# Kernel tuning notes

Hardware: AMD Instinct MI355X
Metric: run time of the kernel (lower is better)

The kernel has to match this reference:

```python
import jax, jax.numpy as jnp
import numpy as np

H = 256
NUM_REL = 460
NUM_ENT = 20000
B = 4096
CUR_TS = 10
PATH_LEN = 8


def _gru_step(x, h, W_ih, W_hh, b_ih, b_hh):
    # PyTorch GRUCell math
    gi = x @ W_ih.T + b_ih          # [B, 3H]
    gh = h @ W_hh.T + b_hh          # [B, 3H]
    ir, iz, inn = jnp.split(gi, 3, axis=1)
    hr, hz, hn = jnp.split(gh, 3, axis=1)
    r = jax.nn.sigmoid(ir + hr)
    z = jax.nn.sigmoid(iz + hz)
    n = jnp.tanh(inn + r * hn)
    return (1.0 - z) * n + z * h


def setup_inputs() -> dict:
    key = jax.random.key(0)
    ks = jax.random.split(key, 24)
    s = 1.0 / np.sqrt(H)
    f32 = jnp.float32
    d = {
        "pre_emb": jax.random.normal(ks[0], (NUM_ENT, H), f32),
        "r_emb": jax.random.normal(ks[1], (NUM_REL, H), f32),
        "partial_embeding": jax.random.normal(ks[2], (B, CUR_TS * NUM_REL), f32),
        # params (uniform-ish linear init scaled by 1/sqrt(H))
        "W_map1": jax.random.normal(ks[3], (2 * H, H), f32) * s,
        "b_map1": jax.random.normal(ks[4], (2 * H,), f32) * s,
        "W_map2": jax.random.normal(ks[5], (H, 2 * H), f32) * s,
        "b_map2": jax.random.normal(ks[6], (H,), f32) * s,
        "W_h1": jax.random.normal(ks[7], (H, H), f32) * s,
        "b_h1": jax.random.normal(ks[8], (H,), f32) * s,
        "W_h2": jax.random.normal(ks[9], (H, H), f32) * s,
        "b_h2": jax.random.normal(ks[10], (H,), f32) * s,
        "W_attn": jax.random.normal(ks[11], (H, H), f32) * s,
        "b_attn": jax.random.normal(ks[12], (H,), f32) * s,
        "W_align": jax.random.normal(ks[13], (H, H), f32) * s,
        "b_align": jax.random.normal(ks[14], (H,), f32) * s,
        "W_ih": jax.random.normal(ks[15], (3 * H, H), f32) * s,
        "W_hh": jax.random.normal(ks[16], (3 * H, H), f32) * s,
        "b_ih": jax.random.normal(ks[17], (3 * H,), f32) * s,
        "b_hh": jax.random.normal(ks[18], (3 * H,), f32) * s,
        "all_triples": jax.random.randint(ks[19], (B, 3), 0, NUM_REL, dtype=jnp.int64)
        if jax.config.jax_enable_x64 else jax.random.randint(ks[19], (B, 3), 0, NUM_REL, dtype=jnp.int32),
        "cur_ts": CUR_TS,
        "num_rel": NUM_REL,
    }
    return d


def reference(pre_emb, r_emb, partial_embeding,
              W_map1, b_map1, W_map2, b_map2,
              W_h1, b_h1, W_h2, b_h2,
              W_attn, b_attn, W_align, b_align,
              W_ih, W_hh, b_ih, b_hh,
              all_triples, cur_ts, num_rel):
    # rel_mapping1 -> rel_mapping2
    mapped_rel = (r_emb @ W_map1.T + b_map1) @ W_map2.T + b_map2     # [R, H]
    q_rel = mapped_rel[all_triples[:, 1]]                            # [B, H]

    # attention logits base (constant over timesteps): linear_attn(q_rel) @ mapped_rel.T
    attn_base = (q_rel @ W_attn.T + b_attn) @ mapped_rel.T           # [B, R]

    start_ts = max(cur_ts - PATH_LEN, 0)
    nb = partial_embeding.shape[0]
    cur_seq = partial_embeding.reshape(nb, cur_ts, num_rel)[:, start_ts:cur_ts]  # [B, T, R]
    cur_seq = jnp.swapaxes(cur_seq, 0, 1)                            # [T, B, R]

    h0 = jnp.zeros((nb, H), dtype=pre_emb.dtype)

    def step(h, cur):
        attn = cur * attn_base
        attn = jnp.where(attn == 0, jnp.asarray(-1e9, attn.dtype), attn)
        attn = jax.nn.softmax(attn, axis=1)
        x = attn @ mapped_rel                                        # [B, H]
        return _gru_step(x, h, W_ih, W_hh, b_ih, b_hh), None

    gru_hidden, _ = jax.lax.scan(step, h0, cur_seq)

    # predicted history embedding + match loss (MSE)
    predicted_hist = 0.1 * ((q_rel @ W_h1.T + b_h1) @ W_h2.T + b_h2) + q_rel
    match_loss = jnp.mean((predicted_hist - gru_hidden) ** 2)

    # forward_forth, distmult scoring
    h2 = _gru_step(q_rel, predicted_hist, W_ih, W_hh, b_ih, b_hh)    # [B, H]
    aligned_all = pre_emb @ W_align.T + b_align                      # [E, H]
    sub = aligned_all[all_triples[:, 0]]                             # [B, H]
    score_logits = (sub * h2) @ aligned_all.T                        # [B, E]
    score = jax.nn.sigmoid(score_logits)

    # BCE(sigmoid(logits), one_hot(obj)) in stable logits form without
    # materializing the dense one-hot label matrix:
    # mean over B*E of [ softplus(x) - x * label ]
    obj = all_triples[:, 2]
    pos_logits = score_logits[jnp.arange(nb), obj]
    path_loss = (jnp.sum(jax.nn.softplus(score_logits)) - jnp.sum(pos_logits)) / (nb * score_logits.shape[1])

    return match_loss, path_loss, score
```

## Files before the change

### kernel.cpp

```cpp
#include <hip/hip_runtime.h>
#include <hip/hip_bf16.h>

typedef __hip_bfloat16 bf16;
typedef __attribute__((ext_vector_type(8))) short short8;
typedef __attribute__((ext_vector_type(4))) float f32x4;
typedef __attribute__((ext_vector_type(4))) short short4v;

#define NREL 460
#define KP   480
#define NENT 20000
#define NENT_PAD 20224
#define NB   4096

__device__ inline float sigmoidf_(float x){ return 1.f/(1.f+__expf(-x)); }

__device__ inline void gload16(const bf16* g, bf16* l){
  __builtin_amdgcn_global_load_lds(
      (const __attribute__((address_space(1))) unsigned int*)g,
      (__attribute__((address_space(3))) unsigned int*)l, 16, 0, 0);
}

__device__ __forceinline__ void fgemm_body(
    const float* __restrict__ A, int lda, int arows,
    const float* __restrict__ B, int ldb,
    const float* __restrict__ bias,
    float* __restrict__ C, int ldc, int K, int mode,
    const float* __restrict__ add_src, bf16* __restrict__ ct_out,
    float* As, float* Bs, int bx, int by)
{
  const int tid = threadIdx.x;
  const int row0 = bx*64, col0 = by*64;
  const int tx = tid & 15, ty = tid >> 4;
  float acc[4][4] = {};
  for (int k0 = 0; k0 < K; k0 += 32){
    __syncthreads();
    #pragma unroll
    for (int s = 0; s < 2; ++s){
      int slot = tid + s*256;
      int r = slot >> 3, c4 = (slot & 7)*4;
      int ra = row0 + r; if (ra >= arows) ra = arows - 1;
      float4 v = *(const float4*)(A + (long)ra*lda + k0 + c4);
      As[(c4+0)*68+r] = v.x; As[(c4+1)*68+r] = v.y; As[(c4+2)*68+r] = v.z; As[(c4+3)*68+r] = v.w;
      float4 w = *(const float4*)(B + (long)(col0 + r)*ldb + k0 + c4);
      Bs[(c4+0)*68+r] = w.x; Bs[(c4+1)*68+r] = w.y; Bs[(c4+2)*68+r] = w.z; Bs[(c4+3)*68+r] = w.w;
    }
    __syncthreads();
    #pragma unroll
    for (int kk = 0; kk < 32; ++kk){
      float4 a4 = *(const float4*)(&As[kk*68 + ty*4]);
      float4 b4 = *(const float4*)(&Bs[kk*68 + tx*4]);
      float av[4] = {a4.x, a4.y, a4.z, a4.w};
      float bv[4] = {b4.x, b4.y, b4.z, b4.w};
      #pragma unroll
      for (int i = 0; i < 4; ++i)
        #pragma unroll
        for (int j = 0; j < 4; ++j) acc[i][j] += av[i]*bv[j];
    }
  }
  const int rb = row0 + ty*4, cb = col0 + tx*4;
  if (mode == 1){
    #pragma unroll
    for (int i = 0; i < 4; ++i){
      float4 v = {acc[i][0], acc[i][1], acc[i][2], acc[i][3]};
      *(float4*)(C + (long)(rb+i)*ldc + cb) = v;
      int rr = rb + i;
      if (rr < KP){
        #pragma unroll
        for (int j = 0; j < 4; ++j)
          ct_out[(cb+j)*KP + rr] = __float2bfloat16(rr < NREL ? acc[i][j] : 0.f);
      }
    }
  } else if (mode == 2){
    #pragma unroll
    for (int i = 0; i < 4; ++i){
      float4 v;
      #pragma unroll
      for (int j = 0; j < 4; ++j)
        ((float*)&v)[j] = 0.1f*(acc[i][j] + bias[cb+j]) + add_src[(long)(rb+i)*ldc + cb+j];
      *(float4*)(C + (long)(rb+i)*ldc + cb) = v;
    }
  } else {
    float bv[4] = {0,0,0,0};
    if (bias){ bv[0]=bias[cb]; bv[1]=bias[cb+1]; bv[2]=bias[cb+2]; bv[3]=bias[cb+3]; }
    #pragma unroll
    for (int i = 0; i < 4; ++i){
      float4 v = {acc[i][0]+bv[0], acc[i][1]+bv[1], acc[i][2]+bv[2], acc[i][3]+bv[3]};
      *(float4*)(C + (long)(rb+i)*ldc + cb) = v;
    }
  }
}

struct FDesc {
  const float* A; const float* B; const float* bias; float* C;
  const float* add; bf16* ct;
  int lda, ldb, ldc, K, arows, mode;
};

template<int MODE>
__device__ __forceinline__ void gemm128_body(
    const bf16* __restrict__ A, int lda,
    const bf16* __restrict__ B, int ldb,
    const float* __restrict__ bias,
    void* __restrict__ C, long ldc,
    int K, int n_valid, double* __restrict__ sp_sum,
    const int* __restrict__ trips,
    bf16* sbuf, float* wsum, int bx, int by)
{
  const int tid = threadIdx.x;
  const int lane = tid & 63, wave = tid >> 6;
  const long row0 = (long)bx * 128;
  const long col0 = (long)by * 128;
  const int sr = tid >> 2;
  const int sc = ((tid & 3) ^ ((sr >> 1) & 3)) * 8;
  const bf16* Ag0 = A + (row0 + sr)*lda + sc;
  const bf16* Ag1 = A + (row0 + 64 + sr)*lda + sc;
  const bf16* Bg0 = B + (col0 + sr)*ldb + sc;
  const bf16* Bg1 = B + (col0 + 64 + sr)*ldb + sc;
  bf16* As_ = sbuf;
  bf16* Bs_ = sbuf + 12288;
  const int wr = (wave >> 1)*64, wc = (wave & 1)*64;
  const int rA = lane & 15;
  const int kA = ((lane >> 4) ^ ((rA >> 1) & 3)) * 8;
  f32x4 acc[4][4] = {};
  const int nt = K >> 5;
  auto stage = [&](int t, int buf){
    const int k0 = t << 5;
    gload16(Ag0 + k0, As_ + buf*4096 + tid*8);
    gload16(Ag1 + k0, As_ + buf*4096 + 2048 + tid*8);
    gload16(Bg0 + k0, Bs_ + buf*4096 + tid*8);
    gload16(Bg1 + k0, Bs_ + buf*4096 + 2048 + tid*8);
  };
  stage(0, 0); stage(1, 1);
  int cur = 0;
  for (int t = 0; t < nt; ++t){
    if (t + 2 < nt){
      int nb = cur + 2; if (nb >= 3) nb -= 3;
      stage(t + 2, nb);
      asm volatile("s_waitcnt vmcnt(8)" ::: "memory");
    } else if (t + 2 == nt){
      asm volatile("s_waitcnt vmcnt(4)" ::: "memory");
    } else {
      asm volatile("s_waitcnt vmcnt(0)" ::: "memory");
    }
    __builtin_amdgcn_s_barrier();
    short8 a[4], b[4];
    #pragma unroll
    for (int m = 0; m < 4; ++m) a[m] = *(const short8*)(As_ + cur*4096 + (wr + m*16 + rA)*32 + kA);
    #pragma unroll
    for (int n = 0; n < 4; ++n) b[n] = *(const short8*)(Bs_ + cur*4096 + (wc + n*16 + rA)*32 + kA);
    asm volatile("s_waitcnt lgkmcnt(0)" ::: "memory");
    __builtin_amdgcn_s_barrier();
    #pragma unroll
    for (int m = 0; m < 4; ++m)
      #pragma unroll
      for (int n = 0; n < 4; ++n)
        acc[m][n] = __builtin_amdgcn_mfma_f32_16x16x32_bf16(a[m], b[n], acc[m][n], 0,0,0);
    if (++cur == 3) cur = 0;
  }
  const int ri = (lane >> 4)*4, ci = lane & 15;
  __syncthreads();
  if constexpr (MODE == 1){
    bf16* epi = sbuf + wave*1152;
    const int rrow = lane >> 2, q = lane & 3;
    #pragma unroll
    for (int m = 0; m < 4; ++m){
      #pragma unroll
      for (int n = 0; n < 4; ++n){
        long c = col0 + wc + n*16 + ci;
        float bv = bias ? bias[c] : 0.f;
        #pragma unroll
        for (int i = 0; i < 4; ++i)
          epi[(ri+i)*72 + n*16 + ci] = __float2bfloat16(acc[m][n][i] + bv);
      }
      long gr = row0 + wr + m*16 + rrow;
      bf16* gp = (bf16*)C + gr*ldc + col0 + wc + q*16;
      const bf16* lp = epi + rrow*72 + q*16;
      *(short8*)(gp)     = *(const short8*)(lp);
      *(short8*)(gp + 8) = *(const short8*)(lp + 8);
    }
  } else {
    float* epi = (float*)sbuf + wave*1088;
    const int rrow = lane >> 2, q = lane & 3;
    const bool maybe = (col0 + wc) < 464;
    float spart = 0.f, ppart = 0.f;
    #pragma unroll
    for (int m = 0; m < 4; ++m){
      int obj[4];
      if (maybe){
        #pragma unroll
        for (int i = 0; i < 4; ++i)
          obj[i] = trips[3*(int)(row0 + wr + m*16 + ri + i) + 2];
      }
      #pragma unroll
      for (int n = 0; n < 4; ++n){
        long c = col0 + wc + n*16 + ci;
        bool cv = (c < n_valid);
        #pragma unroll
        for (int i = 0; i < 4; ++i){
          float v = acc[m][n][i];
          float sg = 0.f;
          if (cv){
            float e = __expf(-fabsf(v));
            float tt = 1.f + e;
            float rr = __builtin_amdgcn_rcpf(tt);
            sg = (v >= 0.f) ? rr : 1.f - rr;
            spart += fmaxf(v, 0.f) + e*(0.9404f - 0.2537f*e);
            if (maybe && c == obj[i]) ppart += v;
          }
          epi[(ri+i)*68 + n*16 + ci + 2] = sg;
        }
      }
      long gr = row0 + wr + m*16 + rrow;
      long c16 = col0 + wc + q*16;
      if (c16 < n_valid){
        float* gp = (float*)C + gr*ldc + c16;
        const float* lp = epi + rrow*68 + q*16 + 2;
        *(float2*)(gp)      = *(const float2*)(lp);
        *(float4*)(gp + 2)  = *(const float4*)(lp + 2);
        *(float4*)(gp + 6)  = *(const float4*)(lp + 6);
        *(float4*)(gp + 10) = *(const float4*)(lp + 10);
        *(float2*)(gp + 14) = *(const float2*)(lp + 14);
      }
    }
    #pragma unroll
    for (int off = 32; off >= 1; off >>= 1){
      spart += __shfl_xor(spart, off);
      ppart += __shfl_xor(ppart, off);
    }
    if (lane == 0){ wsum[wave] = spart; wsum[4+wave] = ppart; }
    __syncthreads();
    if (tid == 0)
      atomicAdd(sp_sum, (double)(wsum[0]+wsum[1]+wsum[2]+wsum[3]));
    if (tid == 1)
      atomicAdd(sp_sum+1, (double)(wsum[4]+wsum[5]+wsum[6]+wsum[7]));
  }
}

__global__ __launch_bounds__(256) void k_conv_g1(
    const float4* __restrict__ s0, short4v* __restrict__ d0, int n0,
    const float4* __restrict__ s1, short4v* __restrict__ d1, int n1,
    const float4* __restrict__ s2, short4v* __restrict__ d2, int n2,
    short4v* __restrict__ pad0, int n3, double* __restrict__ dz,
    const float* __restrict__ gA, const float* __restrict__ gB,
    const float* __restrict__ gbias, float* __restrict__ gC)
{
  __shared__ __align__(16) float As[32*68];
  __shared__ __align__(16) float Bs[32*68];
  int bid = blockIdx.x;
  if (bid < 64){
    fgemm_body(gA,256,NREL, gB,256, gbias, gC,512, 256, 0, nullptr,nullptr,
               As, Bs, bid&7, bid>>3);
    return;
  }
  int i = (bid-64)*256 + threadIdx.x;
  if (i < n0+n1+n2){
    const float4* s; short4v* d; int j;
    if (i < n0){ s = s0; d = d0; j = i; }
    else if (i < n0+n1){ s = s1; d = d1; j = i-n0; }
    else { s = s2; d = d2; j = i-n0-n1; }
    float4 v = s[j];
    bf16 a = __float2bfloat16(v.x), b = __float2bfloat16(v.y);
    bf16 c = __float2bfloat16(v.z), e = __float2bfloat16(v.w);
    short4v o; o.x = *(short*)&a; o.y = *(short*)&b; o.z = *(short*)&c; o.w = *(short*)&e;
    d[j] = o;
  } else if (i < n0+n1+n2+n3){
    short4v z = {0,0,0,0};
    pad0[i - (n0+n1+n2)] = z;
  } else if (i < n0+n1+n2+n3+8){
    dz[i - (n0+n1+n2+n3)] = 0.0;
  }
}

__global__ __launch_bounds__(256) void k_fgemm(
    const float* A, int lda, int arows, const float* B, int ldb,
    const float* bias, float* C, int ldc, int K, int mode,
    const float* add_src, bf16* ct_out){
  __shared__ __align__(16) float As[32*68];
  __shared__ __align__(16) float Bs[32*68];
  fgemm_body(A, lda, arows, B, ldb, bias, C, ldc, K, mode, add_src, ct_out,
             As, Bs, blockIdx.x, blockIdx.y);
}

__global__ __launch_bounds__(256) void k_fgemm_multi(FDesc d0, FDesc d1, FDesc d2,
                                                     int y1, int y2){
  __shared__ __align__(16) float As[32*68];
  __shared__ __align__(16) float Bs[32*68];
  int y = blockIdx.y;
  FDesc d; int by;
  if (y < y1){ d = d0; by = y; }
  else if (y < y2){ d = d1; by = y - y1; }
  else { d = d2; by = y - y2; }
  fgemm_body(d.A, d.lda, d.arows, d.B, d.ldb, d.bias, d.C, d.ldc, d.K, d.mode,
             d.add, d.ct, As, Bs, blockIdx.x, by);
}

__global__ __launch_bounds__(256) void k_g3_aligned(
    FDesc d0, FDesc d1, FDesc d2, int y1, int y2,
    const bf16* __restrict__ pA, const bf16* __restrict__ pB,
    const float* __restrict__ pbias, bf16* __restrict__ pC)
{
  __shared__ __align__(16) char smem[49152 + 32];
  int bid = blockIdx.x;
  if (bid < 160){
    int bx = bid & 7, y = bid >> 3;
    FDesc d; int by;
    if (y < y1){ d = d0; by = y; }
    else if (y < y2){ d = d1; by = y - y1; }
    else { d = d2; by = y - y2; }
    fgemm_body(d.A, d.lda, d.arows, d.B, d.ldb, d.bias, d.C, d.ldc, d.K, d.mode,
               d.add, d.ct, (float*)smem, (float*)(smem + 17408), bx, by);
  } else {
    int idx = bid - 160;
    gemm128_body<1>(pA, 256, pB, 256, pbias, pC, 256, 256, 0, nullptr, nullptr,
                    (bf16*)smem, (float*)(smem + 49152), idx % 158, idx / 158);
  }
}

__global__ __launch_bounds__(256) void k_soft_makep(const float* __restrict__ partial,
    const float* __restrict__ attn_base, const int* __restrict__ trips,
    bf16* __restrict__ attn_all,
    const bf16* __restrict__ Qbf,
    const float* __restrict__ M_ih, const float* __restrict__ ghp,
    const float* __restrict__ ph, const float* __restrict__ b_ih,
    bf16* __restrict__ P){
  int bid = blockIdx.x;
  if (bid >= NB/4){
    int i = (bid - NB/4)*256 + threadIdx.x;
    int b = i >> 8, k = i & 255;
    int s = trips[b*3+0], rel = trips[b*3+1];
    long rb = (long)rel*768;
    float rg = sigmoidf_(M_ih[rb+k]     + b_ih[k]     + ghp[rb+k]);
    float zg = sigmoidf_(M_ih[rb+256+k] + b_ih[256+k] + ghp[rb+256+k]);
    float ng = tanhf    (M_ih[rb+512+k] + b_ih[512+k] + rg*ghp[rb+512+k]);
    float h2v = (1.f - zg)*ng + zg*ph[rel*256+k];
    P[i] = __float2bfloat16(__bfloat162float(Qbf[(long)s*256+k]) * h2v);
    return;
  }
  int wave = threadIdx.x >> 6, lane = threadIdx.x & 63;
  int b = bid*4 + wave;
  int rel = trips[b*3+1];
  const float* base = attn_base + (long)rel*512;
  float bs[8];
  #pragma unroll
  for (int s = 0; s < 8; ++s){
    int idx = s*64 + lane;
    bs[s] = (idx < NREL) ? base[idx] : 0.f;
  }
  const float* cur0 = partial + (long)b*4600 + 2*NREL;
  for (int t = 0; t < 8; ++t){
    const float* cur = cur0 + t*NREL;
    float v[8]; float mx = -1e30f;
    #pragma unroll
    for (int s = 0; s < 8; ++s){
      int idx = s*64 + lane;
      float val = -1e30f;
      if (idx < NREL){
        float pz = cur[idx]*bs[s];
        val = (pz == 0.f) ? -1e9f : pz;
      }
      v[s] = val; mx = fmaxf(mx, val);
    }
    #pragma unroll
    for (int off = 32; off >= 1; off >>= 1) mx = fmaxf(mx, __shfl_xor(mx, off));
    float sum = 0.f;
    #pragma unroll
    for (int s = 0; s < 8; ++s){
      int idx = s*64 + lane;
      if (idx < NREL){ v[s] = __expf(v[s]-mx); sum += v[s]; }
    }
    #pragma unroll
    for (int off = 32; off >= 1; off >>= 1) sum += __shfl_xor(sum, off);
    float inv = 1.f/sum;
    long obase = ((long)t*NB + b)*KP;
    #pragma unroll
    for (int s = 0; s < 8; ++s){
      int idx = s*64 + lane;
      if (idx < KP) attn_all[obase + idx] = __float2bfloat16(idx < NREL ? v[s]*inv : 0.f);
    }
  }
}

__global__ __launch_bounds__(256) void k_gemm_dual(
    const bf16* __restrict__ A2, const bf16* __restrict__ B2,
    void* __restrict__ C2, long ldc2, int K2, int nvalid2,
    double* __restrict__ sp, const int* __restrict__ trips, int nblk2,
    const bf16* __restrict__ A1, const bf16* __restrict__ B1,
    const float* __restrict__ bias1, void* __restrict__ C1, long ldc1, int K1)
{
  __shared__ __align__(16) bf16 sbuf[24576];
  __shared__ float wsum[8];
  int bid = blockIdx.x;
  if (bid < nblk2){
    gemm128_body<2>(A2, 256, B2, 256, nullptr, C2, ldc2, K2, nvalid2, sp, trips,
                    sbuf, wsum, bid & 31, bid >> 5);
  } else {
    int idx = bid - nblk2;
    gemm128_body<1>(A1, KP, B1, KP, bias1, C1, ldc1, K1, 0, nullptr, nullptr,
                    sbuf, wsum, idx & 255, idx >> 8);
  }
}

__global__ __launch_bounds__(512) void k_scan(
    const bf16* __restrict__ gi_all,
    const bf16* __restrict__ W_hh_bf,
    const float* __restrict__ b_hh,
    const float* __restrict__ ph,
    const int* __restrict__ trips,
    double* __restrict__ dsum, int* __restrict__ done, float* __restrict__ outf)
{
  __shared__ __align__(16) bf16 hl[16*264];
  __shared__ __align__(16) bf16 gbuf[2][16*768];
  __shared__ float red[8];
  const int tid = threadIdx.x;
  const int lane = tid & 63, wave = tid >> 6;
  const int brow0 = blockIdx.x * 16;
  const int rA = lane & 15, kA = (lane >> 4) * 8;
  const int ci = lane & 15, rbase = (lane >> 4) * 4;
  float hreg[2][4] = {};
  float bh[3][2];
  #pragma unroll
  for (int f = 0; f < 2; ++f){
    int cf = wave*32 + f*16 + ci;
    bh[0][f] = b_hh[cf]; bh[1][f] = b_hh[256+cf]; bh[2][f] = b_hh[512+cf];
  }
  short8 warr[3][2][6];
  #pragma unroll
  for (int g = 0; g < 3; ++g)
    #pragma unroll
    for (int f = 0; f < 2; ++f)
      #pragma unroll
      for (int k = 0; k < 6; ++k)
        warr[g][f][k] = *(const short8*)(W_hh_bf + (g*256 + wave*32 + f*16 + rA)*256 + k*32 + kA);
  {
    const bf16* src = gi_all + (long)brow0 * 768;
    #pragma unroll
    for (int i = 0; i < 3; ++i){
      int off = (wave*3 + i)*512 + lane*8;
      gload16(src + off, gbuf[0] + off);
    }
  }
  int cur = 0;
  for (int t = 0; t < 8; ++t){
    f32x4 acc[3][2] = {};
    if (t > 0){
      #pragma unroll
      for (int k = 0; k < 8; ++k){
        short8 a = *(const short8*)(hl + rA*264 + k*32 + kA);
        #pragma unroll
        for (int g = 0; g < 3; ++g)
          #pragma unroll
          for (int f = 0; f < 2; ++f){
            short8 b;
            if (k < 6) b = warr[g][f][k];
            else b = *(const short8*)(W_hh_bf + (g*256 + wave*32 + f*16 + rA)*256 + k*32 + kA);
            acc[g][f] = __builtin_amdgcn_mfma_f32_16x16x32_bf16(a, b, acc[g][f], 0,0,0);
          }
      }
    }
    asm volatile("s_waitcnt lgkmcnt(0) vmcnt(0)" ::: "memory");
    __builtin_amdgcn_s_barrier();
    if (t < 7){
      const bf16* src = gi_all + ((long)(t+1)*NB + brow0) * 768;
      bf16* dst = gbuf[cur ^ 1];
      #pragma unroll
      for (int i = 0; i < 3; ++i){
        int off = (wave*3 + i)*512 + lane*8;
        gload16(src + off, dst + off);
      }
    }
    const bf16* gl = gbuf[cur];
    #pragma unroll
    for (int f = 0; f < 2; ++f){
      int cf = wave*32 + f*16 + ci;
      #pragma unroll
      for (int i = 0; i < 4; ++i){
        int rloc = rbase + i;
        float gir = __bfloat162float(gl[rloc*768 + cf]);
        float giz = __bfloat162float(gl[rloc*768 + 256 + cf]);
        float gin = __bfloat162float(gl[rloc*768 + 512 + cf]);
        float rg = sigmoidf_(gir + acc[0][f][i] + bh[0][f]);
        float zg = sigmoidf_(giz + acc[1][f][i] + bh[1][f]);
        float ng = tanhf(gin + rg*(acc[2][f][i] + bh[2][f]));
        float hn = (1.f - zg)*ng + zg*hreg[f][i];
        hreg[f][i] = hn;
        hl[rloc*264 + cf] = __float2bfloat16(hn);
      }
    }
    asm volatile("s_waitcnt lgkmcnt(0)" ::: "memory");
    __builtin_amdgcn_s_barrier();
    cur ^= 1;
  }
  float d = 0.f;
  #pragma unroll
  for (int f = 0; f < 2; ++f){
    int cf = wave*32 + f*16 + ci;
    #pragma unroll
    for (int i = 0; i < 4; ++i){
      int rel = trips[(brow0 + rbase + i)*3 + 1];
      float diff = ph[rel*256 + cf] - hreg[f][i];
      d += diff*diff;
    }
  }
  #pragma unroll
  for (int off = 32; off >= 1; off >>= 1) d += __shfl_xor(d, off);
  if (lane == 0) red[wave] = d;
  __syncthreads();
  if (tid == 0){
    float s = 0.f;
    #pragma unroll
    for (int w = 0; w < 8; ++w) s += red[w];
    atomicAdd(dsum, (double)s);
    asm volatile("s_waitcnt vmcnt(0)" ::: "memory");
    int ticket = atomicAdd(done, 1);
    if (ticket == (int)gridDim.x - 1){
      double m  = atomicAdd(dsum+0, 0.0);
      double sp = atomicAdd(dsum+1, 0.0);
      double pp = atomicAdd(dsum+2, 0.0);
      outf[0] = (float)(m / (4096.0*256.0));
      outf[1] = (float)((sp - pp) / (4096.0*20000.0));
    }
  }
}

extern "C" void kernel_launch(void* const* d_in, const int* in_sizes, int n_in,
                              void* d_out, int out_size, void* d_ws, size_t ws_size,
                              hipStream_t stream){
  const float* pre_emb = (const float*)d_in[0];
  const float* r_emb   = (const float*)d_in[1];
  const float* partial = (const float*)d_in[2];
  const float* W_map1  = (const float*)d_in[3];
  const float* b_map1  = (const float*)d_in[4];
  const float* W_map2  = (const float*)d_in[5];
  const float* b_map2  = (const float*)d_in[6];
  const float* W_h1    = (const float*)d_in[7];
  const float* b_h1    = (const float*)d_in[8];
  const float* W_h2    = (const float*)d_in[9];
  const float* b_h2    = (const float*)d_in[10];
  const float* W_attn  = (const float*)d_in[11];
  const float* b_attn  = (const float*)d_in[12];
  const float* W_align = (const float*)d_in[13];
  const float* b_align = (const float*)d_in[14];
  const float* W_ih    = (const float*)d_in[15];
  const float* W_hh    = (const float*)d_in[16];
  const float* b_ih    = (const float*)d_in[17];
  const float* b_hh    = (const float*)d_in[18];
  const int*   trips   = (const int*)d_in[19];
  float* out = (float*)d_out;

  char* w = (char*)d_ws;
  auto alloc = [&](size_t bytes)->char*{
    char* r = w; w += (bytes + 255) & ~size_t(255); return r;
  };
  double* dsum      = (double*)alloc(128);
  int*    done      = (int*)(dsum + 4);
  float* t1         = (float*)alloc(512*512*4);
  float* mapped     = (float*)alloc(512*256*4);
  float* a1         = (float*)alloc(512*256*4);
  float* th         = (float*)alloc(512*256*4);
  float* ph         = (float*)alloc(512*256*4);
  float* M_ih       = (float*)alloc(512*768*4);
  float* ghp        = (float*)alloc(512*768*4);
  float* attn_base  = (float*)alloc(512*512*4);
  bf16*  M_ihT      = (bf16*)alloc(768*KP*2);
  bf16*  W_hh_bf    = (bf16*)alloc(768*256*2);
  bf16*  W_align_bf = (bf16*)alloc(256*256*2);
  bf16*  Q_bf       = (bf16*)alloc((size_t)NENT_PAD*256*2);
  bf16*  P_bf       = (bf16*)alloc((size_t)NB*256*2);
  bf16*  attn_all   = (bf16*)alloc((size_t)8*NB*KP*2);
  bf16*  gi_all     = (bf16*)alloc((size_t)8*NB*768*2);
  bf16*  pre_bf     = attn_all;

  {
    int n0 = NENT*256/4, n1 = 768*256/4, n2 = 256*256/4;
    int n3 = (NENT_PAD-NENT)*256/4;
    int ntot = n0+n1+n2+n3+8;
    k_conv_g1<<<64 + (ntot+255)/256, 256, 0, stream>>>(
        (const float4*)pre_emb, (short4v*)pre_bf, n0,
        (const float4*)W_hh, (short4v*)W_hh_bf, n1,
        (const float4*)W_align, (short4v*)W_align_bf, n2,
        (short4v*)(pre_bf + (size_t)NENT*256), n3, dsum,
        r_emb, W_map1, b_map1, t1);
  }
  k_fgemm<<<dim3(8,4),256,0,stream>>>(t1,512,512, W_map2,512, b_map2, mapped,256, 512, 0, nullptr, nullptr);
  {
    FDesc d0 = { mapped, W_ih,   nullptr, M_ih, nullptr, M_ihT, 256, 256, 768, 256, 512, 1 };
    FDesc d1 = { mapped, W_attn, b_attn,  a1,   nullptr, nullptr, 256, 256, 256, 256, 512, 0 };
    FDesc d2 = { mapped, W_h1,   b_h1,    th,   nullptr, nullptr, 256, 256, 256, 256, 512, 0 };
    k_g3_aligned<<<160 + 316, 256, 0, stream>>>(d0, d1, d2, 12, 16,
                                                pre_bf, W_align_bf, b_align, Q_bf);
  }
  {
    FDesc d0 = { th, W_h2,   b_h2,    ph,        mapped,  nullptr, 256, 256, 256, 256, 512, 2 };
    FDesc d1 = { a1, mapped, nullptr, attn_base, nullptr, nullptr, 256, 256, 512, 256, 512, 0 };
    k_fgemm_multi<<<dim3(8,12),256,0,stream>>>(d0, d1, d1, 4, 12);
  }
  k_fgemm<<<dim3(8,12),256,0,stream>>>(ph,256,512, W_hh,256, b_hh, ghp,768, 256, 0, nullptr, nullptr);
  k_soft_makep<<<NB/4 + NB,256,0,stream>>>(partial, attn_base, trips, attn_all,
                                           Q_bf, M_ih, ghp, ph, b_ih, P_bf);
  k_gemm_dual<<<5056 + 1536, 256, 0, stream>>>(
      P_bf, Q_bf, out+2, NENT, 256, NENT, dsum+1, trips, 5056,
      attn_all, M_ihT, b_ih, gi_all, 768, KP);
  k_scan<<<NB/16,512,0,stream>>>(gi_all, W_hh_bf, b_hh, ph, trips, dsum, done, out);
}
```

Before: 389.5 us.

## Add specialized score GEMM with full-K A tile in LDS and register-prefetched B

Adds a dedicated score kernel body for the [B,E] distmult logits GEMM. It loads the whole 128x256 A tile into LDS once with an XOR swizzle, and streams B fragments straight from global memory into registers with two-stage prefetch, so the K loop has no per-step LDS staging or barriers. The fused sigmoid, softplus and positive-logit epilogue is kept. LDS use grows to 64KB per block, which may lower occupancy for the other GEMM path sharing the kernel, and B reads from global are uncoalesced per lane and rely on cache.

```diff
diff --git a/kernel.cpp b/kernel.cpp
--- a/kernel.cpp
+++ b/kernel.cpp
@@ -236,6 +236,116 @@
   }
 }
 
+__device__ __forceinline__ void score_body(
+    const bf16* __restrict__ P, const bf16* __restrict__ Q,
+    float* __restrict__ C, long ldc, int n_valid,
+    double* __restrict__ sp_sum, const int* __restrict__ trips,
+    bf16* Alds, float* wsum, int bx, int by)
+{
+  const int tid = threadIdx.x;
+  const int lane = tid & 63, wave = tid >> 6;
+  const long row0 = (long)bx * 128;
+  const long col0 = (long)by * 128;
+  #pragma unroll
+  for (int i = 0; i < 16; ++i){
+    int G = i*256 + tid;
+    int row = G >> 5, gk = G & 31;
+    gload16(P + (row0 + row)*256 + ((gk ^ (row & 7)) << 3), Alds + (size_t)G*8);
+  }
+  asm volatile("s_waitcnt vmcnt(0)" ::: "memory");
+  __builtin_amdgcn_s_barrier();
+  const int wr = (wave >> 1)*64, wc = (wave & 1)*64;
+  const int rA = lane & 15, q4 = lane >> 4, xg = rA & 7;
+  const bf16* B0p = Q + (col0 + wc +  0 + rA)*256 + q4*8;
+  const bf16* B1p = Q + (col0 + wc + 16 + rA)*256 + q4*8;
+  const bf16* B2p = Q + (col0 + wc + 32 + rA)*256 + q4*8;
+  const bf16* B3p = Q + (col0 + wc + 48 + rA)*256 + q4*8;
+  f32x4 acc[4][4] = {};
+  short8 bn1[4], bn2[4];
+  bn1[0] = *(const short8*)(B0p);      bn1[1] = *(const short8*)(B1p);
+  bn1[2] = *(const short8*)(B2p);      bn1[3] = *(const short8*)(B3p);
+  bn2[0] = *(const short8*)(B0p + 32); bn2[1] = *(const short8*)(B1p + 32);
+  bn2[2] = *(const short8*)(B2p + 32); bn2[3] = *(const short8*)(B3p + 32);
+  #pragma unroll
+  for (int t = 0; t < 8; ++t){
+    short8 bc[4];
+    #pragma unroll
+    for (int n = 0; n < 4; ++n){ bc[n] = bn1[n]; bn1[n] = bn2[n]; }
+    if (t + 2 < 8){
+      const int k0 = (t + 2) * 32;
+      bn2[0] = *(const short8*)(B0p + k0); bn2[1] = *(const short8*)(B1p + k0);
+      bn2[2] = *(const short8*)(B2p + k0); bn2[3] = *(const short8*)(B3p + k0);
+    }
+    short8 a[4];
+    #pragma unroll
+    for (int m = 0; m < 4; ++m){
+      int row = wr + m*16 + rA;
+      a[m] = *(const short8*)(Alds + row*256 + (((t*4 + q4) ^ xg) << 3));
+    }
+    #pragma unroll
+    for (int m = 0; m < 4; ++m)
+      #pragma unroll
+      for (int n = 0; n < 4; ++n)
+        acc[m][n] = __builtin_amdgcn_mfma_f32_16x16x32_bf16(a[m], bc[n], acc[m][n], 0,0,0);
+  }
+  const int ri = (lane >> 4)*4, ci = lane & 15;
+  __syncthreads();
+  float* epi = (float*)Alds + wave*1088;
+  const int rrow = lane >> 2, q = lane & 3;
+  const bool maybe = (col0 + wc) < 464;
+  float spart = 0.f, ppart = 0.f;
+  #pragma unroll
+  for (int m = 0; m < 4; ++m){
+    int obj[4];
+    if (maybe){
+      #pragma unroll
+      for (int i = 0; i < 4; ++i)
+        obj[i] = trips[3*(int)(row0 + wr + m*16 + ri + i) + 2];
+    }
+    #pragma unroll
+    for (int n = 0; n < 4; ++n){
+      long c = col0 + wc + n*16 + ci;
+      bool cv = (c < n_valid);
+      #pragma unroll
+      for (int i = 0; i < 4; ++i){
+        float v = acc[m][n][i];
+        float sg = 0.f;
+        if (cv){
+          float e = __expf(-fabsf(v));
+          float tt = 1.f + e;
+          float rr = __builtin_amdgcn_rcpf(tt);
+          sg = (v >= 0.f) ? rr : 1.f - rr;
+          spart += fmaxf(v, 0.f) + e*(0.9404f - 0.2537f*e);
+          if (maybe && c == obj[i]) ppart += v;
+        }
+        epi[(ri+i)*68 + n*16 + ci + 2] = sg;
+      }
+    }
+    long gr = row0 + wr + m*16 + rrow;
+    long c16 = col0 + wc + q*16;
+    if (c16 < n_valid){
+      float* gp = C + gr*ldc + c16;
+      const float* lp = epi + rrow*68 + q*16 + 2;
+      *(float2*)(gp)      = *(const float2*)(lp);
+      *(float4*)(gp + 2)  = *(const float4*)(lp + 2);
+      *(float4*)(gp + 6)  = *(const float4*)(lp + 6);
+      *(float4*)(gp + 10) = *(const float4*)(lp + 10);
+      *(float2*)(gp + 14) = *(const float2*)(lp + 14);
+    }
+  }
+  #pragma unroll
+  for (int off = 32; off >= 1; off >>= 1){
+    spart += __shfl_xor(spart, off);
+    ppart += __shfl_xor(ppart, off);
+  }
+  if (lane == 0){ wsum[wave] = spart; wsum[4+wave] = ppart; }
+  __syncthreads();
+  if (tid == 0)
+    atomicAdd(sp_sum, (double)(wsum[0]+wsum[1]+wsum[2]+wsum[3]));
+  if (tid == 1)
+    atomicAdd(sp_sum+1, (double)(wsum[4]+wsum[5]+wsum[6]+wsum[7]));
+}
+
 __global__ __launch_bounds__(256) void k_conv_g1(
     const float4* __restrict__ s0, short4v* __restrict__ d0, int n0,
     const float4* __restrict__ s1, short4v* __restrict__ d1, int n1,
@@ -387,12 +497,12 @@
     const bf16* __restrict__ A1, const bf16* __restrict__ B1,
     const float* __restrict__ bias1, void* __restrict__ C1, long ldc1, int K1)
 {
-  __shared__ __align__(16) bf16 sbuf[24576];
+  __shared__ __align__(16) bf16 sbuf[32768];
   __shared__ float wsum[8];
   int bid = blockIdx.x;
   if (bid < nblk2){
-    gemm128_body<2>(A2, 256, B2, 256, nullptr, C2, ldc2, K2, nvalid2, sp, trips,
-                    sbuf, wsum, bid & 31, bid >> 5);
+    score_body(A2, B2, (float*)C2, ldc2, nvalid2, sp, trips,
+               sbuf, wsum, bid & 31, bid >> 5);
   } else {
     int idx = bid - nblk2;
     gemm128_body<1>(A1, KP, B1, KP, bias1, C1, ldc1, K1, 0, nullptr, nullptr,
```

Result: slower. 439.3 us (+12.8%).
